# Optimization experiments

Hardware: AMD Instinct MI355X
Metric: run time of the kernel (lower is better)

Reference implementation:

```python
import jax, jax.numpy as jnp
import numpy as np


def haar_dwt2(x):
    """Single-level 2D Haar DWT on last two axes, matching pywt.dwt2('haar').

    x: [..., H, W] with H, W even.
    Returns [..., 4, H/2, W/2] stacked as (LL, LH, HL, HH) where, per pywt,
    LH=cH (highpass along H, lowpass along W), HL=cV, HH=cD.
    """
    B, C, H, W = x.shape
    # group 2x2 blocks: [B, C, H/2, 2, W/2, 2]
    xb = x.reshape(B, C, H // 2, 2, W // 2, 2)
    x00 = xb[:, :, :, 0, :, 0]  # even row, even col
    x01 = xb[:, :, :, 0, :, 1]  # even row, odd col
    x10 = xb[:, :, :, 1, :, 0]  # odd row, even col
    x11 = xb[:, :, :, 1, :, 1]  # odd row, odd col
    half = jnp.asarray(0.5, dtype=x.dtype)
    LL = (x00 + x01 + x10 + x11) * half
    LH = (x00 + x01 - x10 - x11) * half  # cH: detail along rows (H)
    HL = (x00 - x01 + x10 - x11) * half  # cV: detail along cols (W)
    HH = (x00 - x01 - x10 + x11) * half  # cD: detail both axes
    return jnp.stack([LL, LH, HL, HH], axis=1)  # [B, 4, C, H/2, W/2]


def setup_inputs() -> dict:
    key = jax.random.key(0)
    x = jax.random.normal(key, (8, 32, 512, 512), dtype=jnp.float32)
    return {"input": x}


def reference(input):
    return haar_dwt2(input)
```

## Files before the change

kernel.cpp:

```cpp
#include <hip/hip_runtime.h>


#define C_ 32
typedef float v4f __attribute__((ext_vector_type(4)));

__global__ __launch_bounds__(256)
void WaveletTransform_14319420965150_kernel(const float* __restrict__ x,
                                            float* __restrict__ out) {
    __shared__ v4f sd[2][16][64];

    const int bid = blockIdx.x;
    const int bc  = bid >> 5;
    const int h2b = bid & 31;

    const v4f* __restrict__ xin = (const v4f*)x;
    v4f* __restrict__ o         = (v4f*)out;

    const int t    = threadIdx.x;
    const int lane = t & 63;
    const int wid  = t >> 6;

    const size_t imgbase = (size_t)bc * 65536 + (size_t)h2b * (16 * 128);

    v4f a[4], b[4];
    #pragma unroll
    for (int j = 0; j < 4; ++j) {
        const size_t g = imgbase + (size_t)(4 * j + wid) * 128 + 2 * lane;
        a[j] = xin[g];
        b[j] = xin[g + 1];
    }
    #pragma unroll
    for (int j = 0; j < 4; ++j) {
        const int r = 4 * j + wid;
        v4f s = { a[j].x + a[j].y, a[j].z + a[j].w,
                  b[j].x + b[j].y, b[j].z + b[j].w };
        v4f d = { a[j].x - a[j].y, a[j].z - a[j].w,
                  b[j].x - b[j].y, b[j].z - b[j].w };
        sd[0][r][lane] = s;
        sd[1][r][lane] = d;
    }
    __syncthreads();

    const int q = wid;
    const int p = q >> 1;
    const bool neg = (q & 1);
    size_t ob = ((size_t)(bc >> 5) * 128 + (size_t)q * C_ + (bc & (C_ - 1))) * 16384
              + (size_t)(h2b * 8) * 64 + lane;

    #pragma unroll
    for (int r = 0; r < 8; ++r) {
        v4f top = sd[p][2 * r][lane];
        v4f bot = sd[p][2 * r + 1][lane];
        v4f res = neg ? (top - bot) * 0.5f : (top + bot) * 0.5f;
        o[ob + (size_t)r * 64] = res;
    }
}

extern "C" void kernel_launch(void* const* d_in, const int* in_sizes, int n_in,
                              void* d_out, int out_size, void* d_ws, size_t ws_size,
                              hipStream_t stream) {
    const float* x = (const float*)d_in[0];
    float* out = (float*)d_out;
    const int block = 256;
    const int grid  = 8192;
    WaveletTransform_14319420965150_kernel<<<grid, block, 0, stream>>>(x, out);
}
```

Baseline: 426.1 us.

## Make blocks persistent over four tiles and prefetch the next tile's loads

The grid shrinks from 8192 blocks to 2048, and each block now walks four tiles in a loop. While it computes and stores the current tile from shared memory, it issues the global loads for the next tile. Manual barriers and sched_barriers keep that ordering and protect the shared buffer from being overwritten too early. This is meant to hide global load latency behind the store phase, at the cost of more registers, extra barriers and fewer blocks to balance across the GPU.

New measurement: 434.5 us. No clear change (+2.0%).

```diff
diff --git a/kernel.cpp b/kernel.cpp
--- a/kernel.cpp
+++ b/kernel.cpp
@@ -1,7 +1,10 @@
 #include <hip/hip_runtime.h>
 
 
-#define C_ 32
+#define C_    32
+#define NBLK_ 2048
+#define TPB_  4
+
 typedef float v4f __attribute__((ext_vector_type(4)));
 
 __global__ __launch_bounds__(256)
@@ -9,50 +12,89 @@
                                             float* __restrict__ out) {
     __shared__ v4f sd[2][16][64];
 
-    const int bid = blockIdx.x;
-    const int bc  = bid >> 5;
-    const int h2b = bid & 31;
-
     const v4f* __restrict__ xin = (const v4f*)x;
     v4f* __restrict__ o         = (v4f*)out;
 
     const int t    = threadIdx.x;
     const int lane = t & 63;
     const int wid  = t >> 6;
-
-    const size_t imgbase = (size_t)bc * 65536 + (size_t)h2b * (16 * 128);
+    const int q    = wid;
+    const int p    = q >> 1;
+    const bool neg = (q & 1);
 
     v4f a[4], b[4];
-    #pragma unroll
-    for (int j = 0; j < 4; ++j) {
-        const size_t g = imgbase + (size_t)(4 * j + wid) * 128 + 2 * lane;
-        a[j] = xin[g];
-        b[j] = xin[g + 1];
+
+    int tb = blockIdx.x;
+    {
+        const int bc = tb >> 5, h2b = tb & 31;
+        const size_t imgbase = (size_t)bc * 65536 + (size_t)h2b * 2048;
+        #pragma unroll
+        for (int j = 0; j < 4; ++j) {
+            const size_t g = imgbase + (size_t)(4 * j + wid) * 128 + 2 * lane;
+            a[j] = xin[g]; b[j] = xin[g + 1];
+        }
+        #pragma unroll
+        for (int j = 0; j < 4; ++j) {
+            const int r = 4 * j + wid;
+            v4f s = { a[j].x + a[j].y, a[j].z + a[j].w,
+                      b[j].x + b[j].y, b[j].z + b[j].w };
+            v4f d = { a[j].x - a[j].y, a[j].z - a[j].w,
+                      b[j].x - b[j].y, b[j].z - b[j].w };
+            sd[0][r][lane] = s;
+            sd[1][r][lane] = d;
+        }
     }
-    #pragma unroll
-    for (int j = 0; j < 4; ++j) {
-        const int r = 4 * j + wid;
-        v4f s = { a[j].x + a[j].y, a[j].z + a[j].w,
-                  b[j].x + b[j].y, b[j].z + b[j].w };
-        v4f d = { a[j].x - a[j].y, a[j].z - a[j].w,
-                  b[j].x - b[j].y, b[j].z - b[j].w };
-        sd[0][r][lane] = s;
-        sd[1][r][lane] = d;
-    }
-    __syncthreads();
-
-    const int q = wid;
-    const int p = q >> 1;
-    const bool neg = (q & 1);
-    size_t ob = ((size_t)(bc >> 5) * 128 + (size_t)q * C_ + (bc & (C_ - 1))) * 16384
-              + (size_t)(h2b * 8) * 64 + lane;
+    asm volatile("s_waitcnt lgkmcnt(0)" ::: "memory");
+    __builtin_amdgcn_s_barrier();
+    __builtin_amdgcn_sched_barrier(0);
 
     #pragma unroll
-    for (int r = 0; r < 8; ++r) {
-        v4f top = sd[p][2 * r][lane];
-        v4f bot = sd[p][2 * r + 1][lane];
-        v4f res = neg ? (top - bot) * 0.5f : (top + bot) * 0.5f;
-        o[ob + (size_t)r * 64] = res;
+    for (int k = 0; k < TPB_; ++k) {
+        const int tb_next = tb + NBLK_;
+
+        if (k < TPB_ - 1) {
+            const int bc = tb_next >> 5, h2b = tb_next & 31;
+            const size_t imgbase = (size_t)bc * 65536 + (size_t)h2b * 2048;
+            #pragma unroll
+            for (int j = 0; j < 4; ++j) {
+                const size_t g = imgbase + (size_t)(4 * j + wid) * 128 + 2 * lane;
+                a[j] = xin[g]; b[j] = xin[g + 1];
+            }
+            __builtin_amdgcn_sched_barrier(0);
+        }
+
+        {
+            const int bc = tb >> 5, h2b = tb & 31;
+            size_t ob = ((size_t)(bc >> 5) * 128 + (size_t)q * C_ + (bc & (C_ - 1))) * 16384
+                      + (size_t)(h2b * 8) * 64 + lane;
+            #pragma unroll
+            for (int r = 0; r < 8; ++r) {
+                v4f top = sd[p][2 * r][lane];
+                v4f bot = sd[p][2 * r + 1][lane];
+                v4f res = neg ? (top - bot) * 0.5f : (top + bot) * 0.5f;
+                o[ob + (size_t)r * 64] = res;
+            }
+        }
+
+        if (k < TPB_ - 1) {
+            __builtin_amdgcn_sched_barrier(0);
+            __builtin_amdgcn_s_barrier();
+            __builtin_amdgcn_sched_barrier(0);
+            #pragma unroll
+            for (int j = 0; j < 4; ++j) {
+                const int r = 4 * j + wid;
+                v4f s = { a[j].x + a[j].y, a[j].z + a[j].w,
+                          b[j].x + b[j].y, b[j].z + b[j].w };
+                v4f d = { a[j].x - a[j].y, a[j].z - a[j].w,
+                          b[j].x - b[j].y, b[j].z - b[j].w };
+                sd[0][r][lane] = s;
+                sd[1][r][lane] = d;
+            }
+            asm volatile("s_waitcnt lgkmcnt(0)" ::: "memory");
+            __builtin_amdgcn_s_barrier();
+            __builtin_amdgcn_sched_barrier(0);
+        }
+        tb = tb_next;
     }
 }
 
@@ -62,6 +104,5 @@
     const float* x = (const float*)d_in[0];
     float* out = (float*)d_out;
     const int block = 256;
-    const int grid  = 8192;
-    WaveletTransform_14319420965150_kernel<<<grid, block, 0, stream>>>(x, out);
+    WaveletTransform_14319420965150_kernel<<<NBLK_, block, 0, stream>>>(x, out);
 }
```
